# Kernel optimization log

Hardware: AMD Instinct MI355X
Metric: run time of the kernel (lower is better)

The kernel has to match this reference:

```python
import jax, jax.numpy as jnp
import numpy as np

D_MODEL = 1024
N_HEADS = 16
D_K = D_MODEL // N_HEADS
SCALE = 1.0 / np.sqrt(D_K).astype(np.float32)
NEG = -1000000000.0


def setup_inputs() -> dict:
    key = jax.random.key(0)
    ks = jax.random.split(key, 5)
    B, S = 2, 2048
    query = jax.random.normal(ks[0], (B, S, D_MODEL), dtype=jnp.float32)
    k_in = jax.random.normal(ks[1], (B, S, D_MODEL), dtype=jnp.float32)
    v_in = jax.random.normal(ks[2], (B, S, D_MODEL), dtype=jnp.float32)
    # causal mask, broadcast over batch and heads; 0 entries get -1e9
    mask = jnp.tril(jnp.ones((S, S), dtype=jnp.int32))[None, None, :, :]
    w_qkv = jax.random.normal(ks[3], (D_MODEL, 3 * D_MODEL), dtype=jnp.float32) * (1.0 / np.sqrt(D_MODEL))
    w_o = jax.random.normal(ks[4], (D_MODEL, D_MODEL), dtype=jnp.float32) * (1.0 / np.sqrt(D_MODEL))
    return {"query": query, "key": k_in, "value": v_in, "mask": mask, "w_qkv": w_qkv, "w_o": w_o}


def reference(query, key, value, mask, w_qkv, w_o):
    # NOTE: original module ignores `key`/`value`; q,k,v all come from `query`.
    B, S, _ = query.shape
    qkv = query @ w_qkv                       # [B,S,3D]
    q, k, v = jnp.split(qkv, 3, axis=-1)
    def heads(x):
        return x.reshape(B, S, N_HEADS, D_K).transpose(0, 2, 1, 3)  # [B,H,S,dk]
    Q, K, V = heads(q), heads(k), heads(v)
    scores = jnp.einsum('bhqd,bhkd->bhqk', Q, K) * SCALE            # [B,H,S,S]
    scores = jnp.where(mask == 0, NEG, scores)
    attn = jax.nn.softmax(scores, axis=-1)
    # Dropout(0.1) treated as eval-mode identity for a deterministic reference.
    context = jnp.einsum('bhqk,bhkd->bhqd', attn, V)                # [B,H,S,dk]
    context = context.transpose(0, 2, 1, 3).reshape(B, S, D_MODEL)
    return context @ w_o
```

## Files before the change

### kernel.cpp

```cpp
#include <hip/hip_runtime.h>
#include <stdint.h>


typedef __attribute__((ext_vector_type(8))) short bf16x8;
typedef __attribute__((ext_vector_type(4))) float f32x4;

#define LOG2E 1.44269504088896340736f
#define QSCALE (0.125f * LOG2E)

__device__ __forceinline__ unsigned short f2b(float f) {
  union { float f; unsigned int i; } x; x.f = f;
  unsigned int i = x.i;
  return (unsigned short)((i + 0x7FFFu + ((i >> 16) & 1u)) >> 16);
}

__device__ __forceinline__ void async16(const void* g, void* l) {
  __builtin_amdgcn_global_load_lds(
      (__attribute__((address_space(1))) void*)g,
      (__attribute__((address_space(3))) void*)l, 16, 0, 0);
}

__device__ __forceinline__ f32x4 mfma16(bf16x8 a, bf16x8 b, f32x4 c) {
  return __builtin_amdgcn_mfma_f32_16x16x32_bf16(a, b, c, 0, 0, 0);
}

__device__ __forceinline__ unsigned int fbits(float f) {
  union { float f; unsigned int i; } x; x.f = f;
  return x.i;
}

__global__ __launch_bounds__(256) void prep(
    const float* __restrict__ X, const float* __restrict__ Wqkv,
    const float* __restrict__ Wo, unsigned short* __restrict__ Xb,
    unsigned short* __restrict__ WqkvT, unsigned short* __restrict__ WoT) {
  __shared__ __align__(16) unsigned short Lt[64 * 64];
  const int bx = blockIdx.x;
  const int t = threadIdx.x;
  if (bx < 2048) {
    const size_t i = ((size_t)bx * 256 + t) * 8;
    float4 a = *(const float4*)(X + i);
    float4 b = *(const float4*)(X + i + 4);
    unsigned short e[8];
    e[0] = f2b(a.x); e[1] = f2b(a.y); e[2] = f2b(a.z); e[3] = f2b(a.w);
    e[4] = f2b(b.x); e[5] = f2b(b.y); e[6] = f2b(b.z); e[7] = f2b(b.w);
    *(uint4*)(Xb + i) = *(const uint4*)e;
    return;
  }
  const bool is_qkv = (bx < 2816);
  const int bid = is_qkv ? bx - 2048 : bx - 2816;
  const float* src = is_qkv ? Wqkv : Wo;
  unsigned short* dst = is_qkv ? WqkvT : WoT;
  const int Ccols = is_qkv ? 3072 : 1024;
  const int r0 = (bid & 15) * 64, c0 = (bid >> 4) * 64;
  const float s = (is_qkv && c0 < 1024) ? QSCALE : 1.0f;
#pragma unroll
  for (int it = 0; it < 4; ++it) {
    int c = it * 256 + t;
    int sr = c >> 4, co = (c & 15) * 4;
    float4 v = *(const float4*)(src + (size_t)(r0 + sr) * Ccols + c0 + co);
    Lt[(co + 0) * 64 + sr] = f2b(v.x * s);
    Lt[(co + 1) * 64 + sr] = f2b(v.y * s);
    Lt[(co + 2) * 64 + sr] = f2b(v.z * s);
    Lt[(co + 3) * 64 + sr] = f2b(v.w * s);
  }
  __syncthreads();
#pragma unroll
  for (int it = 0; it < 2; ++it) {
    int c = it * 256 + t;
    int dr = c >> 3, so = (c & 7) * 8;
    *(uint4*)(dst + (size_t)(c0 + dr) * 1024 + r0 + so) =
        *(const uint4*)(Lt + dr * 64 + so);
  }
}

__global__ __launch_bounds__(256) void gemm_qkv(
    const unsigned short* __restrict__ A, const unsigned short* __restrict__ Bt,
    unsigned short* __restrict__ C, unsigned short* __restrict__ Vt) {
  constexpr int K = 1024, N = 3072;
  __shared__ __align__(16) unsigned short Sm[16896];
  unsigned short* As = Sm;
  unsigned short* Bs = Sm + 8192;
  unsigned short* Lt = Sm;

  const int t = threadIdx.x;
  const int w = t >> 6, l = t & 63;
  const int flat = blockIdx.x + 24 * blockIdx.y;
  const int swz = (flat & 7) * 96 + (flat >> 3);
  const int m0 = (swz / 24) * 128, n0 = (swz % 24) * 128;
  const int wm = (w >> 1) * 64, wn = (w & 1) * 64;
  const int lrow = l & 15, lq = l >> 4;

  f32x4 acc[4][4] = {};

  for (int k0 = 0; k0 < K; k0 += 64) {
    __syncthreads();
#pragma unroll
    for (int r = 0; r < 4; ++r) {
      const int c = r * 256 + t;
      const int row = c >> 3;
      const int so = ((c & 7) ^ (row & 7)) * 8;
      async16(A + (size_t)(m0 + row) * K + k0 + so,
              As + (size_t)(r * 256 + t) * 8);
      async16(Bt + (size_t)(n0 + row) * K + k0 + so,
              Bs + (size_t)(r * 256 + t) * 8);
    }
    asm volatile("s_waitcnt vmcnt(0)" ::: "memory");
    __syncthreads();

#pragma unroll
    for (int kh = 0; kh < 2; ++kh) {
      bf16x8 af[4], bf[4];
      const int phys = ((kh * 4 + lq) ^ (lrow & 7)) * 8;
#pragma unroll
      for (int i = 0; i < 4; ++i)
        af[i] = *(const bf16x8*)(As + (wm + i * 16 + lrow) * 64 + phys);
#pragma unroll
      for (int j = 0; j < 4; ++j)
        bf[j] = *(const bf16x8*)(Bs + (wn + j * 16 + lrow) * 64 + phys);
#pragma unroll
      for (int i = 0; i < 4; ++i)
#pragma unroll
        for (int j = 0; j < 4; ++j)
          acc[i][j] = mfma16(af[i], bf[j], acc[i][j]);
    }
  }

  if (n0 < 2048) {
#pragma unroll
    for (int i = 0; i < 4; ++i)
#pragma unroll
      for (int j = 0; j < 4; ++j)
#pragma unroll
        for (int r = 0; r < 4; ++r) {
          int gr = m0 + wm + i * 16 + lq * 4 + r;
          int gc = n0 + wn + j * 16 + lrow;
          C[(size_t)gr * N + gc] = f2b(acc[i][j][r]);
        }
  } else {
    __syncthreads();
#pragma unroll
    for (int i = 0; i < 4; ++i)
#pragma unroll
      for (int j = 0; j < 4; ++j) {
        int col_loc = wn + j * 16 + lrow;
        int row_loc = wm + i * 16 + lq * 4;
        uint2 pk;
        pk.x = (unsigned int)f2b(acc[i][j][0]) |
               ((unsigned int)f2b(acc[i][j][1]) << 16);
        pk.y = (unsigned int)f2b(acc[i][j][2]) |
               ((unsigned int)f2b(acc[i][j][3]) << 16);
        *(uint2*)(Lt + col_loc * 132 + row_loc) = pk;
      }
    __syncthreads();
    const int b = m0 >> 11, s0 = m0 & 2047;
    const int vb0 = n0 - 2048;
#pragma unroll
    for (int rnd = 0; rnd < 8; ++rnd) {
      int vrow = rnd * 16 + (t >> 4);
      int sloc = (t & 15) * 8;
      int vcol = vb0 + vrow;
      int bh = b * 16 + (vcol >> 6);
      int d = vcol & 63;
      *(uint4*)(Vt + ((size_t)bh * 64 + d) * 2048 + s0 + sloc) =
          *(const uint4*)(Lt + vrow * 132 + sloc);
    }
  }
}

__global__ __launch_bounds__(256) void gemm_o(
    const unsigned short* __restrict__ A, const unsigned short* __restrict__ Bt,
    float* __restrict__ C, int M, int N, int K) {
  __shared__ __align__(16) unsigned short As[128 * 64];
  __shared__ __align__(16) unsigned short Bs[128 * 64];
  const int t = threadIdx.x;
  const int w = t >> 6, l = t & 63;
  const int flat = blockIdx.x + 8 * blockIdx.y;
  const int swz = (flat & 7) * 32 + (flat >> 3);
  const int m0 = (swz >> 3) * 128, n0 = (swz & 7) * 128;
  const int wm = (w >> 1) * 64, wn = (w & 1) * 64;
  const int lrow = l & 15, lq = l >> 4;

  f32x4 acc[4][4] = {};

  for (int k0 = 0; k0 < K; k0 += 64) {
    __syncthreads();
#pragma unroll
    for (int r = 0; r < 4; ++r) {
      const int c = r * 256 + t;
      const int row = c >> 3;
      const int so = ((c & 7) ^ (row & 7)) * 8;
      async16(A + (size_t)(m0 + row) * K + k0 + so,
              As + (size_t)(r * 256 + t) * 8);
      async16(Bt + (size_t)(n0 + row) * K + k0 + so,
              Bs + (size_t)(r * 256 + t) * 8);
    }
    asm volatile("s_waitcnt vmcnt(0)" ::: "memory");
    __syncthreads();

#pragma unroll
    for (int kh = 0; kh < 2; ++kh) {
      bf16x8 af[4], bf[4];
      const int phys = ((kh * 4 + lq) ^ (lrow & 7)) * 8;
#pragma unroll
      for (int i = 0; i < 4; ++i)
        af[i] = *(const bf16x8*)(As + (wm + i * 16 + lrow) * 64 + phys);
#pragma unroll
      for (int j = 0; j < 4; ++j)
        bf[j] = *(const bf16x8*)(Bs + (wn + j * 16 + lrow) * 64 + phys);
#pragma unroll
      for (int i = 0; i < 4; ++i)
#pragma unroll
        for (int j = 0; j < 4; ++j)
          acc[i][j] = mfma16(af[i], bf[j], acc[i][j]);
    }
  }

#pragma unroll
  for (int i = 0; i < 4; ++i)
#pragma unroll
    for (int j = 0; j < 4; ++j)
#pragma unroll
      for (int r = 0; r < 4; ++r) {
        int gr = m0 + wm + i * 16 + lq * 4 + r;
        int gc = n0 + wn + j * 16 + lrow;
        C[(size_t)gr * N + gc] = acc[i][j][r];
      }
}

__global__ __launch_bounds__(512, 4) void attn_fwd(
    const unsigned short* __restrict__ qkv,
    const unsigned short* __restrict__ Vt,
    unsigned short* __restrict__ ctx) {
  __shared__ __align__(16) unsigned short Ks[2][64 * 64];
  __shared__ __align__(16) unsigned short Vs[2][64 * 64];
  __shared__ __align__(16) unsigned short Ps[8][16 * 72];

  const int bh = blockIdx.x;
  const int ti = 31 - blockIdx.y;
  const int b = bh >> 4, h = bh & 15;
  const int t = threadIdx.x;
  const int g = t >> 8;
  const int tl = t & 255;
  const int w = tl >> 6;
  const int gw = t >> 6;
  const int l = t & 63;
  const int lm = l & 15, lq = l >> 4;
  const int sw = lm & 7;
  const int c0 = (lq ^ sw) * 8;
  const int c1 = ((lq + 4) ^ sw) * 8;

  const unsigned short* Qp = qkv + (size_t)(b * 2048) * 3072 + h * 64;
  const unsigned short* Kp = qkv + (size_t)(b * 2048) * 3072 + 1024 + h * 64;
  const unsigned short* Vb = Vt + (size_t)bh * 64 * 2048;

  const int qrow = ti * 64 + w * 16 + lm;
  bf16x8 qf0 = *(const bf16x8*)(Qp + (size_t)qrow * 3072 + lq * 8);
  bf16x8 qf1 = *(const bf16x8*)(Qp + (size_t)qrow * 3072 + 32 + lq * 8);

  bf16x8 vones;
#pragma unroll
  for (int j = 0; j < 8; ++j) vones[j] = (short)0x3F80;

  const int srow = tl >> 3, scp = tl & 7;
  const int sso = (scp ^ (srow & 7)) * 8;
  const unsigned short* kp0 = Kp + (size_t)(g * 64 + srow) * 3072 + sso;
  const unsigned short* kp1 = kp0 + (size_t)32 * 3072;
  const unsigned short* vp0 = Vb + (size_t)srow * 2048 + g * 64 + sso;
  const unsigned short* vp1 = vp0 + (size_t)32 * 2048;
  unsigned short* kd0 = Ks[g] + (size_t)(w * 64) * 8;
  unsigned short* kd1 = Ks[g] + (size_t)(256 + w * 64) * 8;
  unsigned short* vd0 = Vs[g] + (size_t)(w * 64) * 8;
  unsigned short* vd1 = Vs[g] + (size_t)(256 + w * 64) * 8;

  f32x4 oacc[4] = {};
  f32x4 lacc = {};

  const int nsup = (ti >> 1) + 1;

  for (int jj = 0; jj < nsup; ++jj) {
    const int kt = 2 * jj + g;
    const bool have = (kt <= ti);
    __syncthreads();
    if (have) {
      async16(kp0, kd0);
      async16(vp0, vd0);
      async16(kp1, kd1);
      async16(vp1, vd1);
    }
    kp0 += 128 * 3072; kp1 += 128 * 3072;
    vp0 += 128; vp1 += 128;
    asm volatile("s_waitcnt vmcnt(0)" ::: "memory");
    __syncthreads();
    if (!have) continue;

    const unsigned short* Kc = Ks[g];
    const unsigned short* Vc = Vs[g];

    bf16x8 vf[8];
#pragma unroll
    for (int nt = 0; nt < 4; ++nt) {
      const unsigned short* vr = Vc + (nt * 16 + lm) * 64;
      vf[nt] = *(const bf16x8*)(vr + c0);
      vf[4 + nt] = *(const bf16x8*)(vr + c1);
    }

    f32x4 sacc[4] = {};
    __builtin_amdgcn_s_setprio(1);
#pragma unroll
    for (int mt = 0; mt < 4; ++mt) {
      const unsigned short* kr = Kc + (mt * 16 + lm) * 64;
      bf16x8 bk0 = *(const bf16x8*)(kr + c0);
      bf16x8 bk1 = *(const bf16x8*)(kr + c1);
      sacc[mt] = mfma16(bk0, qf0, sacc[mt]);
      sacc[mt] = mfma16(bk1, qf1, sacc[mt]);
    }
    __builtin_amdgcn_s_setprio(0);

    const bool diag = (kt == ti);
    const int qloc = w * 16 + lm;
#pragma unroll
    for (int mt = 0; mt < 4; ++mt) {
      float p0 = __builtin_amdgcn_exp2f(sacc[mt][0]);
      float p1 = __builtin_amdgcn_exp2f(sacc[mt][1]);
      float p2 = __builtin_amdgcn_exp2f(sacc[mt][2]);
      float p3 = __builtin_amdgcn_exp2f(sacc[mt][3]);
      if (diag) {
        const int kvb = mt * 16 + lq * 4;
        if (kvb + 0 > qloc) p0 = 0.f;
        if (kvb + 1 > qloc) p1 = 0.f;
        if (kvb + 2 > qloc) p2 = 0.f;
        if (kvb + 3 > qloc) p3 = 0.f;
      }
      uint2 pk;
      asm("v_cvt_pk_bf16_f32 %0, %1, %2" : "=v"(pk.x) : "v"(p0), "v"(p1));
      asm("v_cvt_pk_bf16_f32 %0, %1, %2" : "=v"(pk.y) : "v"(p2), "v"(p3));
      *(uint2*)(&Ps[gw][lm * 72 + mt * 16 + lq * 4]) = pk;
    }
    asm volatile("s_waitcnt lgkmcnt(0)" ::: "memory");

    __builtin_amdgcn_s_setprio(1);
#pragma unroll
    for (int ks = 0; ks < 2; ++ks) {
      bf16x8 pa = *(const bf16x8*)(&Ps[gw][lm * 72 + ks * 32 + lq * 8]);
#pragma unroll
      for (int nt = 0; nt < 4; ++nt)
        oacc[nt] = mfma16(pa, vf[ks * 4 + nt], oacc[nt]);
      lacc = mfma16(pa, vones, lacc);
    }
    __builtin_amdgcn_s_setprio(0);
  }

  __syncthreads();
  float* fbuf = (float*)Ks;
  float* lbuf = (float*)Ps;
  if (g == 1) {
#pragma unroll
    for (int nt = 0; nt < 4; ++nt)
#pragma unroll
      for (int r = 0; r < 4; ++r)
        fbuf[(w * 16 + lq * 4 + r) * 64 + nt * 16 + lm] = oacc[nt][r];
    if (lm == 0) {
#pragma unroll
      for (int r = 0; r < 4; ++r) lbuf[w * 16 + lq * 4 + r] = lacc[r];
    }
  }
  __syncthreads();
  if (g == 0) {
    float rinv[4];
#pragma unroll
    for (int r = 0; r < 4; ++r)
      rinv[r] = 1.f / (lacc[r] + lbuf[w * 16 + lq * 4 + r]);
#pragma unroll
    for (int nt = 0; nt < 4; ++nt)
#pragma unroll
      for (int r = 0; r < 4; ++r) {
        float v = oacc[nt][r] +
                  fbuf[(w * 16 + lq * 4 + r) * 64 + nt * 16 + lm];
        size_t tok = (size_t)b * 2048 + ti * 64 + w * 16 + lq * 4 + r;
        ctx[tok * 1024 + h * 64 + nt * 16 + lm] = f2b(v * rinv[r]);
      }
  }
}

extern "C" void kernel_launch(void* const* d_in, const int* in_sizes, int n_in,
                              void* d_out, int out_size, void* d_ws,
                              size_t ws_size, hipStream_t stream) {
  const float* query = (const float*)d_in[0];
  const float* w_qkv = (const float*)d_in[4];
  const float* w_o = (const float*)d_in[5];
  float* out = (float*)d_out;

  unsigned short* ws = (unsigned short*)d_ws;
  unsigned short* wqkvT = ws;
  unsigned short* woT = wqkvT + (size_t)3072 * 1024;
  unsigned short* Xb = woT + (size_t)1024 * 1024;
  unsigned short* qkv = Xb + (size_t)4096 * 1024;
  unsigned short* Vt = qkv + (size_t)4096 * 3072;
  unsigned short* ctx = Xb;

  prep<<<dim3(3072), 256, 0, stream>>>(query, w_qkv, w_o, Xb, wqkvT, woT);
  gemm_qkv<<<dim3(24, 32), 256, 0, stream>>>(Xb, wqkvT, qkv, Vt);
  attn_fwd<<<dim3(32, 32), 512, 0, stream>>>(qkv, Vt, ctx);
  gemm_o<<<dim3(8, 32), 256, 0, stream>>>(ctx, woT, out, 4096, 1024, 1024);
}
```

Before: 198.0 us.

## Halve attention block to 256 threads with each wave handling 32 query rows

The attention kernel goes from 512 to 256 threads per block. Each wave now processes two 16-row query sub-tiles, so every K and V fragment read from LDS feeds two MFMAs instead of one. V fragments are loaded inside the PV loop rather than preloaded, and each thread issues four async copies per tile instead of two. This cuts LDS read traffic per FLOP and the thread count per block, at the cost of more registers per wave (launch bounds now 256,3), fewer waves available to hide latency, and more global-to-LDS copies per thread.

```diff
diff --git a/kernel.cpp b/kernel.cpp
--- a/kernel.cpp
+++ b/kernel.cpp
@@ -227,22 +227,22 @@
       }
 }
 
-__global__ __launch_bounds__(512, 4) void attn_fwd(
+__global__ __launch_bounds__(256, 3) void attn_fwd(
     const unsigned short* __restrict__ qkv,
     const unsigned short* __restrict__ Vt,
     unsigned short* __restrict__ ctx) {
   __shared__ __align__(16) unsigned short Ks[2][64 * 64];
   __shared__ __align__(16) unsigned short Vs[2][64 * 64];
-  __shared__ __align__(16) unsigned short Ps[8][16 * 72];
+  __shared__ __align__(16) unsigned short Ps[4][2][16 * 72];
 
   const int bh = blockIdx.x;
   const int ti = 31 - blockIdx.y;
   const int b = bh >> 4, h = bh & 15;
   const int t = threadIdx.x;
-  const int g = t >> 8;
-  const int tl = t & 255;
-  const int w = tl >> 6;
-  const int gw = t >> 6;
+  const int g = t >> 7;
+  const int gl = t & 127;
+  const int w = t >> 6;
+  const int qs = (w & 1) * 32;
   const int l = t & 63;
   const int lm = l & 15, lq = l >> 4;
   const int sw = lm & 7;
@@ -253,27 +253,29 @@
   const unsigned short* Kp = qkv + (size_t)(b * 2048) * 3072 + 1024 + h * 64;
   const unsigned short* Vb = Vt + (size_t)bh * 64 * 2048;
 
-  const int qrow = ti * 64 + w * 16 + lm;
-  bf16x8 qf0 = *(const bf16x8*)(Qp + (size_t)qrow * 3072 + lq * 8);
-  bf16x8 qf1 = *(const bf16x8*)(Qp + (size_t)qrow * 3072 + 32 + lq * 8);
+  bf16x8 qf[2][2];
+#pragma unroll
+  for (int qh = 0; qh < 2; ++qh) {
+    const int qrow = ti * 64 + qs + qh * 16 + lm;
+    qf[qh][0] = *(const bf16x8*)(Qp + (size_t)qrow * 3072 + lq * 8);
+    qf[qh][1] = *(const bf16x8*)(Qp + (size_t)qrow * 3072 + 32 + lq * 8);
+  }
 
   bf16x8 vones;
 #pragma unroll
   for (int j = 0; j < 8; ++j) vones[j] = (short)0x3F80;
 
-  const int srow = tl >> 3, scp = tl & 7;
+  const int srow = gl >> 3, scp = gl & 7;
   const int sso = (scp ^ (srow & 7)) * 8;
-  const unsigned short* kp0 = Kp + (size_t)(g * 64 + srow) * 3072 + sso;
-  const unsigned short* kp1 = kp0 + (size_t)32 * 3072;
-  const unsigned short* vp0 = Vb + (size_t)srow * 2048 + g * 64 + sso;
-  const unsigned short* vp1 = vp0 + (size_t)32 * 2048;
-  unsigned short* kd0 = Ks[g] + (size_t)(w * 64) * 8;
-  unsigned short* kd1 = Ks[g] + (size_t)(256 + w * 64) * 8;
-  unsigned short* vd0 = Vs[g] + (size_t)(w * 64) * 8;
-  unsigned short* vd1 = Vs[g] + (size_t)(256 + w * 64) * 8;
-
-  f32x4 oacc[4] = {};
-  f32x4 lacc = {};
+  const unsigned short* kb = Kp + (size_t)srow * 3072 + sso;
+  const unsigned short* vbp = Vb + (size_t)srow * 2048 + sso;
+  unsigned short* kdst = Ks[g] + (size_t)gl * 8;
+  unsigned short* vdst = Vs[g] + (size_t)gl * 8;
+  size_t koff = (size_t)(g * 64) * 3072;
+  size_t voff = (size_t)(g * 64);
+
+  f32x4 oacc[2][4] = {};
+  f32x4 lacc[2] = {};
 
   const int nsup = (ti >> 1) + 1;
 
@@ -282,13 +284,14 @@
     const bool have = (kt <= ti);
     __syncthreads();
     if (have) {
-      async16(kp0, kd0);
-      async16(vp0, vd0);
-      async16(kp1, kd1);
-      async16(vp1, vd1);
-    }
-    kp0 += 128 * 3072; kp1 += 128 * 3072;
-    vp0 += 128; vp1 += 128;
+#pragma unroll
+      for (int p = 0; p < 4; ++p) {
+        async16(kb + koff + (size_t)(p * 16) * 3072, kdst + p * 1024);
+        async16(vbp + voff + (size_t)(p * 16) * 2048, vdst + p * 1024);
+      }
+    }
+    koff += (size_t)128 * 3072;
+    voff += 128;
     asm volatile("s_waitcnt vmcnt(0)" ::: "memory");
     __syncthreads();
     if (!have) continue;
@@ -296,56 +299,59 @@
     const unsigned short* Kc = Ks[g];
     const unsigned short* Vc = Vs[g];
 
-    bf16x8 vf[8];
-#pragma unroll
-    for (int nt = 0; nt < 4; ++nt) {
-      const unsigned short* vr = Vc + (nt * 16 + lm) * 64;
-      vf[nt] = *(const bf16x8*)(vr + c0);
-      vf[4 + nt] = *(const bf16x8*)(vr + c1);
-    }
-
-    f32x4 sacc[4] = {};
+    f32x4 sacc[2][4] = {};
     __builtin_amdgcn_s_setprio(1);
 #pragma unroll
     for (int mt = 0; mt < 4; ++mt) {
       const unsigned short* kr = Kc + (mt * 16 + lm) * 64;
       bf16x8 bk0 = *(const bf16x8*)(kr + c0);
       bf16x8 bk1 = *(const bf16x8*)(kr + c1);
-      sacc[mt] = mfma16(bk0, qf0, sacc[mt]);
-      sacc[mt] = mfma16(bk1, qf1, sacc[mt]);
+      sacc[0][mt] = mfma16(bk0, qf[0][0], sacc[0][mt]);
+      sacc[0][mt] = mfma16(bk1, qf[0][1], sacc[0][mt]);
+      sacc[1][mt] = mfma16(bk0, qf[1][0], sacc[1][mt]);
+      sacc[1][mt] = mfma16(bk1, qf[1][1], sacc[1][mt]);
     }
     __builtin_amdgcn_s_setprio(0);
 
     const bool diag = (kt == ti);
-    const int qloc = w * 16 + lm;
-#pragma unroll
-    for (int mt = 0; mt < 4; ++mt) {
-      float p0 = __builtin_amdgcn_exp2f(sacc[mt][0]);
-      float p1 = __builtin_amdgcn_exp2f(sacc[mt][1]);
-      float p2 = __builtin_amdgcn_exp2f(sacc[mt][2]);
-      float p3 = __builtin_amdgcn_exp2f(sacc[mt][3]);
-      if (diag) {
-        const int kvb = mt * 16 + lq * 4;
-        if (kvb + 0 > qloc) p0 = 0.f;
-        if (kvb + 1 > qloc) p1 = 0.f;
-        if (kvb + 2 > qloc) p2 = 0.f;
-        if (kvb + 3 > qloc) p3 = 0.f;
-      }
-      uint2 pk;
-      asm("v_cvt_pk_bf16_f32 %0, %1, %2" : "=v"(pk.x) : "v"(p0), "v"(p1));
-      asm("v_cvt_pk_bf16_f32 %0, %1, %2" : "=v"(pk.y) : "v"(p2), "v"(p3));
-      *(uint2*)(&Ps[gw][lm * 72 + mt * 16 + lq * 4]) = pk;
+#pragma unroll
+    for (int qh = 0; qh < 2; ++qh) {
+      const int qloc = qs + qh * 16 + lm;
+#pragma unroll
+      for (int mt = 0; mt < 4; ++mt) {
+        float p0 = __builtin_amdgcn_exp2f(sacc[qh][mt][0]);
+        float p1 = __builtin_amdgcn_exp2f(sacc[qh][mt][1]);
+        float p2 = __builtin_amdgcn_exp2f(sacc[qh][mt][2]);
+        float p3 = __builtin_amdgcn_exp2f(sacc[qh][mt][3]);
+        if (diag) {
+          const int kvb = mt * 16 + lq * 4;
+          if (kvb + 0 > qloc) p0 = 0.f;
+          if (kvb + 1 > qloc) p1 = 0.f;
+          if (kvb + 2 > qloc) p2 = 0.f;
+          if (kvb + 3 > qloc) p3 = 0.f;
+        }
+        uint2 pk;
+        asm("v_cvt_pk_bf16_f32 %0, %1, %2" : "=v"(pk.x) : "v"(p0), "v"(p1));
+        asm("v_cvt_pk_bf16_f32 %0, %1, %2" : "=v"(pk.y) : "v"(p2), "v"(p3));
+        *(uint2*)(&Ps[w][qh][lm * 72 + mt * 16 + lq * 4]) = pk;
+      }
     }
     asm volatile("s_waitcnt lgkmcnt(0)" ::: "memory");
 
     __builtin_amdgcn_s_setprio(1);
 #pragma unroll
     for (int ks = 0; ks < 2; ++ks) {
-      bf16x8 pa = *(const bf16x8*)(&Ps[gw][lm * 72 + ks * 32 + lq * 8]);
-#pragma unroll
-      for (int nt = 0; nt < 4; ++nt)
-        oacc[nt] = mfma16(pa, vf[ks * 4 + nt], oacc[nt]);
-      lacc = mfma16(pa, vones, lacc);
+      bf16x8 pa0 = *(const bf16x8*)(&Ps[w][0][lm * 72 + ks * 32 + lq * 8]);
+      bf16x8 pa1 = *(const bf16x8*)(&Ps[w][1][lm * 72 + ks * 32 + lq * 8]);
+#pragma unroll
+      for (int nt = 0; nt < 4; ++nt) {
+        const unsigned short* vr = Vc + (nt * 16 + lm) * 64;
+        bf16x8 vfr = *(const bf16x8*)(vr + (ks == 0 ? c0 : c1));
+        oacc[0][nt] = mfma16(pa0, vfr, oacc[0][nt]);
+        oacc[1][nt] = mfma16(pa1, vfr, oacc[1][nt]);
+      }
+      lacc[0] = mfma16(pa0, vones, lacc[0]);
+      lacc[1] = mfma16(pa1, vones, lacc[1]);
     }
     __builtin_amdgcn_s_setprio(0);
   }
@@ -355,30 +361,37 @@
   float* lbuf = (float*)Ps;
   if (g == 1) {
 #pragma unroll
-    for (int nt = 0; nt < 4; ++nt)
-#pragma unroll
-      for (int r = 0; r < 4; ++r)
-        fbuf[(w * 16 + lq * 4 + r) * 64 + nt * 16 + lm] = oacc[nt][r];
-    if (lm == 0) {
-#pragma unroll
-      for (int r = 0; r < 4; ++r) lbuf[w * 16 + lq * 4 + r] = lacc[r];
+    for (int qh = 0; qh < 2; ++qh) {
+      const int qq = qs + qh * 16 + lq * 4;
+#pragma unroll
+      for (int nt = 0; nt < 4; ++nt)
+#pragma unroll
+        for (int r = 0; r < 4; ++r)
+          fbuf[(qq + r) * 64 + nt * 16 + lm] = oacc[qh][nt][r];
+      if (lm == 0) {
+#pragma unroll
+        for (int r = 0; r < 4; ++r) lbuf[qq + r] = lacc[qh][r];
+      }
     }
   }
   __syncthreads();
   if (g == 0) {
-    float rinv[4];
-#pragma unroll
-    for (int r = 0; r < 4; ++r)
-      rinv[r] = 1.f / (lacc[r] + lbuf[w * 16 + lq * 4 + r]);
-#pragma unroll
-    for (int nt = 0; nt < 4; ++nt)
-#pragma unroll
-      for (int r = 0; r < 4; ++r) {
-        float v = oacc[nt][r] +
-                  fbuf[(w * 16 + lq * 4 + r) * 64 + nt * 16 + lm];
-        size_t tok = (size_t)b * 2048 + ti * 64 + w * 16 + lq * 4 + r;
-        ctx[tok * 1024 + h * 64 + nt * 16 + lm] = f2b(v * rinv[r]);
-      }
+#pragma unroll
+    for (int qh = 0; qh < 2; ++qh) {
+      const int qq = qs + qh * 16 + lq * 4;
+      float rinv[4];
+#pragma unroll
+      for (int r = 0; r < 4; ++r)
+        rinv[r] = 1.f / (lacc[qh][r] + lbuf[qq + r]);
+#pragma unroll
+      for (int nt = 0; nt < 4; ++nt)
+#pragma unroll
+        for (int r = 0; r < 4; ++r) {
+          float v = oacc[qh][nt][r] + fbuf[(qq + r) * 64 + nt * 16 + lm];
+          size_t tok = (size_t)b * 2048 + ti * 64 + qq + r;
+          ctx[tok * 1024 + h * 64 + nt * 16 + lm] = f2b(v * rinv[r]);
+        }
+    }
   }
 }
 
@@ -400,6 +413,6 @@
 
   prep<<<dim3(3072), 256, 0, stream>>>(query, w_qkv, w_o, Xb, wqkvT, woT);
   gemm_qkv<<<dim3(24, 32), 256, 0, stream>>>(Xb, wqkvT, qkv, Vt);
-  attn_fwd<<<dim3(32, 32), 512, 0, stream>>>(qkv, Vt, ctx);
+  attn_fwd<<<dim3(32, 32), 256, 0, stream>>>(qkv, Vt, ctx);
   gemm_o<<<dim3(8, 32), 256, 0, stream>>>(ctx, woT, out, 4096, 1024, 1024);
 }
```

Measured after the change: 196.3 us. About the same (-0.8%).
